# Kernel tuning notes

Hardware: AMD Instinct MI355X
Metric: run time of the kernel (lower is better)

The kernel has to match this reference:

```python
import jax, jax.numpy as jnp
import numpy as np

B, S, DIM = 4, 4096, 1024
H, HD = 16, 64  # n_heads, head_dim = dim // n_heads
UMV = 20.0      # unified_max_value (init kwarg)


def setup_inputs() -> dict:
    key = jax.random.key(0)
    kx, kw = jax.random.split(key)
    x = jax.random.normal(kx, (B, S, DIM), dtype=jnp.float32)
    # qkv_proj: Linear(dim, 3*dim). Small weight scale + positive bias keeps
    # attention scores inside the keep-window [0, 2*UMV] so denominators are safe.
    W_qkv = jax.random.normal(kw, (DIM, 3 * DIM), dtype=jnp.float32) * 0.02
    b_qkv = jnp.full((3 * DIM,), 0.5, dtype=jnp.float32)
    return {"x": x, "W_qkv": W_qkv, "b_qkv": b_qkv}


def reference(x, W_qkv, b_qkv):
    Bb, Ss, _ = x.shape
    qkv = x @ W_qkv + b_qkv                      # [B,S,3*dim]
    qkv = qkv.reshape(Bb, Ss, H, 3 * HD)          # [B,S,H,3*hd]
    Q, K, V = jnp.split(qkv, 3, axis=-1)          # each [B,S,H,hd]
    # matmul(Q, K.transpose(-2,-1)) on [B,S,H,hd]: contract head_dim -> [B,S,H,H]
    s = jnp.einsum('bshd,bsgd->bshg', Q, K) - UMV
    e = jnp.exp(s)
    mask = (s > UMV) | (s < -UMV)                 # keep only s in [-UMV, UMV]
    e = jnp.where(mask, 0.0, e)
    denom = jnp.sum(e, axis=-1, keepdims=True)
    p = e / denom                                  # [B,S,H,H]
    out = jnp.einsum('bshg,bsgd->bshd', p, V)      # [B,S,H,hd]
    return out
```

## Files before the change

kernel.cpp:

```cpp
#include <hip/hip_runtime.h>

typedef _Float16 v8h __attribute__((ext_vector_type(8)));
typedef _Float16 v4h __attribute__((ext_vector_type(4)));
typedef _Float16 v2h __attribute__((ext_vector_type(2)));
typedef float v4f __attribute__((ext_vector_type(4)));

__device__ __forceinline__ void gl16(const void* g, void* l) {
    __builtin_amdgcn_global_load_lds(
        (const __attribute__((address_space(1))) unsigned int*)g,
        (__attribute__((address_space(3))) unsigned int*)l, 16, 0, 0);
}

__device__ __forceinline__ void wave_lds_fence() {
    asm volatile("s_waitcnt lgkmcnt(0)" ::: "memory");
}

__global__ __launch_bounds__(256) void k_cvt(const float* __restrict__ x,
                                             _Float16* __restrict__ x16,
                                             const float* __restrict__ W,
                                             _Float16* __restrict__ Wt) {
    if (blockIdx.x < 8192) {
        int i = (blockIdx.x * 256 + threadIdx.x) * 8;
        float4 a = *(const float4*)(x + i);
        float4 b = *(const float4*)(x + i + 4);
        v8h h;
        h[0] = (_Float16)a.x; h[1] = (_Float16)a.y; h[2] = (_Float16)a.z; h[3] = (_Float16)a.w;
        h[4] = (_Float16)b.x; h[5] = (_Float16)b.y; h[6] = (_Float16)b.z; h[7] = (_Float16)b.w;
        *(v8h*)(x16 + i) = h;
    } else {
        __shared__ float T[64][68];
        int bid = blockIdx.x - 8192;
        int k0 = (bid & 15) * 64;
        int n0 = (bid >> 4) * 64;
        int t = threadIdx.x;
        int tr = t >> 4;
        int tc = t & 15;
#pragma unroll
        for (int rr = 0; rr < 4; rr++) {
            int kk = rr * 16 + tr;
            float4 v = *(const float4*)(W + (size_t)(k0 + kk) * 3072 + n0 + tc * 4);
            T[kk][tc * 4 + 0] = v.x; T[kk][tc * 4 + 1] = v.y;
            T[kk][tc * 4 + 2] = v.z; T[kk][tc * 4 + 3] = v.w;
        }
        __syncthreads();
#pragma unroll
        for (int ww = 0; ww < 4; ww++) {
            int nn = ww * 16 + tr;
            v4h h;
#pragma unroll
            for (int i = 0; i < 4; i++) h[i] = (_Float16)T[tc * 4 + i][nn];
            *(v4h*)(Wt + (size_t)(n0 + nn) * 1024 + k0 + tc * 4) = h;
        }
    }
}

__global__ __launch_bounds__(256) void k_gemm(const _Float16* __restrict__ A,
                                              const _Float16* __restrict__ Bt,
                                              const float* __restrict__ bias,
                                              _Float16* __restrict__ C) {
    __shared__ __align__(16) _Float16 As[128 * 32];
    __shared__ __align__(16) _Float16 Bs[128 * 32];
    int bm = blockIdx.x & 127;
    int bn = blockIdx.x >> 7;
    int m0 = bm * 128, n0 = bn * 128;
    int tid = threadIdx.x;
    int w = tid >> 6, lane = tid & 63;
    int quad = lane >> 4, l15 = lane & 15;
    int wm = (w & 1) * 64, wn = (w >> 1) * 64;

    int mc1 = w * 16 + (lane >> 2);
    int mc2 = (w + 4) * 16 + (lane >> 2);
    int k8 = (lane & 3) * 8;
    const _Float16* aS1 = A + (size_t)(m0 + mc1) * 1024 + k8;
    const _Float16* aS2 = A + (size_t)(m0 + mc2) * 1024 + k8;
    const _Float16* bS1 = Bt + (size_t)(n0 + mc1) * 1024 + k8;
    const _Float16* bS2 = Bt + (size_t)(n0 + mc2) * 1024 + k8;
    _Float16* lA1 = &As[w * 512];
    _Float16* lA2 = &As[(w + 4) * 512];
    _Float16* lB1 = &Bs[w * 512];
    _Float16* lB2 = &Bs[(w + 4) * 512];

    v4f acc[4][4] = {};

    for (int kt = 0; kt < 1024; kt += 32) {
        __syncthreads();
        gl16(aS1 + kt, lA1);
        gl16(aS2 + kt, lA2);
        gl16(bS1 + kt, lB1);
        gl16(bS2 + kt, lB2);
        __syncthreads();
        v8h af[4], bf[4];
#pragma unroll
        for (int mi = 0; mi < 4; mi++)
            af[mi] = *(const v8h*)&As[(wm + mi * 16 + l15) * 32 + quad * 8];
#pragma unroll
        for (int ni = 0; ni < 4; ni++)
            bf[ni] = *(const v8h*)&Bs[(wn + ni * 16 + l15) * 32 + quad * 8];
#pragma unroll
        for (int mi = 0; mi < 4; mi++)
#pragma unroll
            for (int ni = 0; ni < 4; ni++)
                acc[mi][ni] = __builtin_amdgcn_mfma_f32_16x16x32_f16(af[mi], bf[ni], acc[mi][ni], 0, 0, 0);
    }

#pragma unroll
    for (int ni = 0; ni < 4; ni++) {
        int n = n0 + wn + ni * 16 + l15;
        float bv = bias[n];
#pragma unroll
        for (int mi = 0; mi < 4; mi++) {
            int mbase = m0 + wm + mi * 16 + quad * 4;
#pragma unroll
            for (int r = 0; r < 4; r++)
                C[(size_t)(mbase + r) * 3072 + n] = (_Float16)(acc[mi][ni][r] + bv);
        }
    }
}

__global__ __launch_bounds__(256) void k_attn(const _Float16* __restrict__ qkv,
                                              float* __restrict__ out) {
    __shared__ __align__(16) _Float16 Pb[4][16 * 24];
    int tid = threadIdx.x;
    int w = tid >> 6, lane = tid & 63;
    int pos = blockIdx.x * 4 + w;
    _Float16* P = Pb[w];
    const _Float16* src = qkv + (size_t)pos * 3072;
    int l15 = lane & 15, quad = lane >> 4;

    const _Float16* hrow = src + l15 * 192;
    v8h a0 = *(const v8h*)(hrow + quad * 8);
    v8h a1 = *(const v8h*)(hrow + 32 + quad * 8);
    v8h b0 = *(const v8h*)(hrow + 64 + quad * 8);
    v8h b1 = *(const v8h*)(hrow + 96 + quad * 8);
    int dl = lane & 15;
    v4h vseg[16];
#pragma unroll
    for (int g = 0; g < 16; g++)
        vseg[g] = *(const v4h*)(src + g * 192 + 128 + dl * 4);

    {
        v4f s = {};
        s = __builtin_amdgcn_mfma_f32_16x16x32_f16(a0, b0, s, 0, 0, 0);
        s = __builtin_amdgcn_mfma_f32_16x16x32_f16(a1, b1, s, 0, 0, 0);
        float e4[4];
#pragma unroll
        for (int r = 0; r < 4; r++) {
            float sv = s[r] - 20.0f;
            e4[r] = (sv > 20.0f || sv < -20.0f) ? 0.0f : __expf(sv);
        }
#pragma unroll
        for (int r = 0; r < 4; r++) {
            float t = e4[r];
            t += __shfl_xor(t, 1, 64);
            t += __shfl_xor(t, 2, 64);
            t += __shfl_xor(t, 4, 64);
            t += __shfl_xor(t, 8, 64);
            P[(quad * 4 + r) * 24 + l15] = (_Float16)(e4[r] / t);
        }
    }
    wave_lds_fence();

    {
        v8h p0[4], p1[4];
#pragma unroll
        for (int t = 0; t < 4; t++) {
            const _Float16* Pr = P + (4 * t + quad) * 24;
            p0[t] = *(const v8h*)Pr;
            p1[t] = *(const v8h*)(Pr + 8);
        }
        v2h o[4][2] = {};
#pragma unroll
        for (int g = 0; g < 16; g++) {
            v2h va; va[0] = vseg[g][0]; va[1] = vseg[g][1];
            v2h vb; vb[0] = vseg[g][2]; vb[1] = vseg[g][3];
#pragma unroll
            for (int t = 0; t < 4; t++) {
                _Float16 ph = (g < 8) ? p0[t][g] : p1[t][g - 8];
                v2h p2; p2[0] = ph; p2[1] = ph;
                o[t][0] = p2 * va + o[t][0];
                o[t][1] = p2 * vb + o[t][1];
            }
        }
        float* dst = out + (size_t)pos * 1024;
#pragma unroll
        for (int t = 0; t < 4; t++) {
            float4 v;
            v.x = (float)o[t][0][0];
            v.y = (float)o[t][0][1];
            v.z = (float)o[t][1][0];
            v.w = (float)o[t][1][1];
            *(float4*)(dst + t * 256 + lane * 4) = v;
        }
    }
}

extern "C" void kernel_launch(void* const* d_in, const int* in_sizes, int n_in,
                              void* d_out, int out_size, void* d_ws, size_t ws_size,
                              hipStream_t stream) {
    (void)in_sizes; (void)n_in; (void)out_size; (void)ws_size;
    const float* x  = (const float*)d_in[0];
    const float* Wq = (const float*)d_in[1];
    const float* bq = (const float*)d_in[2];
    float* out = (float*)d_out;

    char* ob = (char*)d_out;
    _Float16* x16   = (_Float16*)ob;
    _Float16* wt16  = (_Float16*)(ob + (48u << 20));
    _Float16* qkv16 = (_Float16*)d_ws;

    k_cvt<<<8960, 256, 0, stream>>>(x, x16, Wq, wt16);
    k_gemm<<<3072, 256, 0, stream>>>(x16, wt16, bq, qkv16);
    k_attn<<<4096, 256, 0, stream>>>(qkv16, out);
}
```

Baseline: 274.4 us.

## Rewrite QKV GEMM as 256x256 tile double-buffered pipelined kernel

Replaces the 128x128, BK=32 single-buffered GEMM with 256x256 tiles of 512 threads, BK=64, and double-buffered LDS. Global-to-LDS loads are interleaved with the MFMA phases under explicit vmcnt waits and barriers, and s_setprio is used around the MFMA bursts. LDS rows are XOR-swizzled to avoid bank conflicts, and block IDs are remapped so that neighbouring blocks share L2 data. The aim is to hide load latency and raise arithmetic intensity, at the cost of heavy register and LDS pressure (about 128KB LDS per block) and fragile hand-tuned wait counts.

```diff
diff --git a/kernel.cpp b/kernel.cpp
--- a/kernel.cpp
+++ b/kernel.cpp
@@ -54,53 +54,112 @@
     }
 }
 
-__global__ __launch_bounds__(256) void k_gemm(const _Float16* __restrict__ A,
-                                              const _Float16* __restrict__ Bt,
-                                              const float* __restrict__ bias,
-                                              _Float16* __restrict__ C) {
-    __shared__ __align__(16) _Float16 As[128 * 32];
-    __shared__ __align__(16) _Float16 Bs[128 * 32];
-    int bm = blockIdx.x & 127;
-    int bn = blockIdx.x >> 7;
-    int m0 = bm * 128, n0 = bn * 128;
+
+#define MFMA16(q, A0K0, A0K1, A1K0, A1K1)                                                   \
+    _Pragma("unroll")                                                                       \
+    for (int ni = 0; ni < 4; ni++) {                                                        \
+        acc[2*(q)][ni]   = __builtin_amdgcn_mfma_f32_16x16x32_f16(A0K0, bf[ni][0], acc[2*(q)][ni], 0, 0, 0);   \
+        acc[2*(q)][ni]   = __builtin_amdgcn_mfma_f32_16x16x32_f16(A0K1, bf[ni][1], acc[2*(q)][ni], 0, 0, 0);   \
+        acc[2*(q)+1][ni] = __builtin_amdgcn_mfma_f32_16x16x32_f16(A1K0, bf[ni][0], acc[2*(q)+1][ni], 0, 0, 0); \
+        acc[2*(q)+1][ni] = __builtin_amdgcn_mfma_f32_16x16x32_f16(A1K1, bf[ni][1], acc[2*(q)+1][ni], 0, 0, 0); \
+    }
+
+#define PHASE(XB, q, PRE, WAIT)                                                             \
+    {                                                                                       \
+        v8h a0k0 = *(const v8h*)&XB[aoff + (2*(q)) * 1024];                                 \
+        v8h a0k1 = *(const v8h*)&XB[(aoff ^ 32) + (2*(q)) * 1024];                          \
+        v8h a1k0 = *(const v8h*)&XB[aoff + (2*(q)+1) * 1024];                               \
+        v8h a1k1 = *(const v8h*)&XB[(aoff ^ 32) + (2*(q)+1) * 1024];                        \
+        PRE                                                                                 \
+        __builtin_amdgcn_s_barrier();                                                       \
+        __builtin_amdgcn_s_setprio(1);                                                      \
+        MFMA16(q, a0k0, a0k1, a1k0, a1k1)                                                   \
+        __builtin_amdgcn_s_setprio(0);                                                      \
+        WAIT                                                                                \
+        __builtin_amdgcn_s_barrier();                                                       \
+    }
+
+#define LOADB(XB)                                                                           \
+    _Pragma("unroll")                                                                       \
+    for (int ni = 0; ni < 4; ni++) {                                                        \
+        bf[ni][0] = *(const v8h*)&XB[boff + ni * 1024];                                     \
+        bf[ni][1] = *(const v8h*)&XB[(boff ^ 32) + ni * 1024];                              \
+    }
+
+#define STAGE_A(t, h, j) gl16(aS + (size_t)((h) * 128 + (j) * 8) * 1024 + (t) * 64,         \
+                              &As[(t) & 1][((h) * 128 + ldsRow + (j) * 8) * 64])
+#define STAGE_B(t, h, j) gl16(bS + (size_t)((h) * 128 + (j) * 8) * 1024 + (t) * 64,         \
+                              &Bs[(t) & 1][((h) * 128 + ldsRow + (j) * 8) * 64])
+
+__global__ __launch_bounds__(512, 2) void k_gemm(const _Float16* __restrict__ A,
+                                                 const _Float16* __restrict__ Bt,
+                                                 const float* __restrict__ bias,
+                                                 _Float16* __restrict__ C) {
+    __shared__ __align__(16) _Float16 As[2][256 * 64];
+    __shared__ __align__(16) _Float16 Bs[2][256 * 64];
+
+    int wg = blockIdx.x;
+    wg = (wg & 7) * 96 + (wg >> 3);
+    int bm = wg / 12, bn = wg % 12;
+    int m0 = bm * 256, n0 = bn * 256;
+
     int tid = threadIdx.x;
-    int w = tid >> 6, lane = tid & 63;
-    int quad = lane >> 4, l15 = lane & 15;
-    int wm = (w & 1) * 64, wn = (w >> 1) * 64;
-
-    int mc1 = w * 16 + (lane >> 2);
-    int mc2 = (w + 4) * 16 + (lane >> 2);
-    int k8 = (lane & 3) * 8;
-    const _Float16* aS1 = A + (size_t)(m0 + mc1) * 1024 + k8;
-    const _Float16* aS2 = A + (size_t)(m0 + mc2) * 1024 + k8;
-    const _Float16* bS1 = Bt + (size_t)(n0 + mc1) * 1024 + k8;
-    const _Float16* bS2 = Bt + (size_t)(n0 + mc2) * 1024 + k8;
-    _Float16* lA1 = &As[w * 512];
-    _Float16* lA2 = &As[(w + 4) * 512];
-    _Float16* lB1 = &Bs[w * 512];
-    _Float16* lB2 = &Bs[(w + 4) * 512];
-
-    v4f acc[4][4] = {};
-
-    for (int kt = 0; kt < 1024; kt += 32) {
-        __syncthreads();
-        gl16(aS1 + kt, lA1);
-        gl16(aS2 + kt, lA2);
-        gl16(bS1 + kt, lB1);
-        gl16(bS2 + kt, lB2);
-        __syncthreads();
-        v8h af[4], bf[4];
-#pragma unroll
-        for (int mi = 0; mi < 4; mi++)
-            af[mi] = *(const v8h*)&As[(wm + mi * 16 + l15) * 32 + quad * 8];
-#pragma unroll
-        for (int ni = 0; ni < 4; ni++)
-            bf[ni] = *(const v8h*)&Bs[(wn + ni * 16 + l15) * 32 + quad * 8];
-#pragma unroll
-        for (int mi = 0; mi < 4; mi++)
-#pragma unroll
-            for (int ni = 0; ni < 4; ni++)
-                acc[mi][ni] = __builtin_amdgcn_mfma_f32_16x16x32_f16(af[mi], bf[ni], acc[mi][ni], 0, 0, 0);
+    int w = tid >> 6;
+    int lane = tid & 63;
+    int l15 = lane & 15, quad = lane >> 4;
+    int wm = (w >> 2) * 128;
+    int wn = (w & 3) * 64;
+
+    int rl = lane >> 3;
+    int ksw = ((lane & 7) ^ rl) * 8;
+    const _Float16* aS = A  + (size_t)(m0 + w * 16 + rl) * 1024 + ksw;
+    const _Float16* bS = Bt + (size_t)(n0 + w * 16 + rl) * 1024 + ksw;
+    int ldsRow = w * 16;
+
+    int swz = (quad ^ (l15 & 7)) * 8;
+    int aoff = (wm + l15) * 64 + swz;
+    int boff = (wn + l15) * 64 + swz;
+
+    v4f acc[8][4] = {};
+    v8h bf[4][2];
+
+    STAGE_A(0, 0, 0); STAGE_A(0, 0, 1); STAGE_A(0, 1, 0); STAGE_A(0, 1, 1);
+    STAGE_B(0, 0, 0); STAGE_B(0, 0, 1); STAGE_B(0, 1, 0); STAGE_B(0, 1, 1);
+    STAGE_A(1, 0, 0); STAGE_A(1, 0, 1); STAGE_A(1, 1, 0); STAGE_A(1, 1, 1);
+    STAGE_B(1, 0, 0); STAGE_B(1, 0, 1); STAGE_B(1, 1, 0); STAGE_B(1, 1, 1);
+    asm volatile("s_waitcnt vmcnt(8)" ::: "memory");
+    __builtin_amdgcn_s_barrier();
+
+    for (int it = 0; it < 8; ++it) {
+        int t = it * 2;
+        LOADB(Bs[0])
+        PHASE(As[0], 0,
+              if (it >= 1) { STAGE_A(t + 1, 0, 0); STAGE_A(t + 1, 0, 1); },
+              )
+        PHASE(As[0], 1,
+              if (it >= 1) { STAGE_A(t + 1, 1, 0); STAGE_A(t + 1, 1, 1); }
+              if (it <= 6) { STAGE_B(t + 2, 0, 0); STAGE_B(t + 2, 0, 1); },
+              )
+        PHASE(As[0], 2,
+              if (it <= 6) { STAGE_B(t + 2, 1, 0); STAGE_B(t + 2, 1, 1); },
+              )
+        PHASE(As[0], 3,
+              ,
+              if (it == 7) { asm volatile("s_waitcnt vmcnt(0)" ::: "memory"); }
+              else         { asm volatile("s_waitcnt vmcnt(4)" ::: "memory"); })
+        LOADB(Bs[1])
+        PHASE(As[1], 0,
+              if (it <= 6) { STAGE_A(t + 2, 0, 0); STAGE_A(t + 2, 0, 1); },
+              )
+        PHASE(As[1], 1,
+              if (it <= 6) { STAGE_A(t + 2, 1, 0); STAGE_A(t + 2, 1, 1); },
+              )
+        PHASE(As[1], 2,
+              if (it <= 6) { STAGE_B(t + 3, 0, 0); STAGE_B(t + 3, 0, 1); },
+              )
+        PHASE(As[1], 3,
+              if (it <= 6) { STAGE_B(t + 3, 1, 0); STAGE_B(t + 3, 1, 1); },
+              if (it <= 6) { asm volatile("s_waitcnt vmcnt(4)" ::: "memory"); })
     }
 
 #pragma unroll
@@ -108,7 +167,7 @@
         int n = n0 + wn + ni * 16 + l15;
         float bv = bias[n];
 #pragma unroll
-        for (int mi = 0; mi < 4; mi++) {
+        for (int mi = 0; mi < 8; mi++) {
             int mbase = m0 + wm + mi * 16 + quad * 4;
 #pragma unroll
             for (int r = 0; r < 4; r++)
@@ -209,6 +268,6 @@
     _Float16* qkv16 = (_Float16*)d_ws;
 
     k_cvt<<<8960, 256, 0, stream>>>(x, x16, Wq, wt16);
-    k_gemm<<<3072, 256, 0, stream>>>(x16, wt16, bq, qkv16);
+    k_gemm<<<768, 512, 0, stream>>>(x16, wt16, bq, qkv16);
     k_attn<<<4096, 256, 0, stream>>>(qkv16, out);
 }
```

Measured after the change: 264.0 us. 3.8% less time.
